# Kernel optimization log

Hardware: AMD Instinct MI355X
Metric: run time of the kernel (lower is better)

## Reference

```python
import jax, jax.numpy as jnp
import numpy as np

EPS_LN = 1e-5
EPS_SUM = 1e-5


def setup_inputs() -> dict:
    key = jax.random.key(0)
    ks = jax.random.split(key, 6)
    B, T, F, D = 8, 1024, 512, 64
    x = jax.random.normal(ks[0], (B, T, F), dtype=jnp.float32)
    state = jnp.zeros((B, 1, D * D), dtype=jnp.float32)
    s = 1.0 / np.sqrt(F)
    Wk = jax.random.uniform(ks[1], (F, D), jnp.float32, -s, s)
    Wq = jax.random.uniform(ks[2], (F, D), jnp.float32, -s, s)
    Wv = jax.random.uniform(ks[3], (F, D), jnp.float32, -s, s)
    gamma = jnp.ones((F,), jnp.float32)
    beta = jnp.zeros((F,), jnp.float32)
    return {"x": x, "state": state, "Wk": Wk, "Wq": Wq, "Wv": Wv,
            "gamma": gamma, "beta": beta}


def _layernorm(x, gamma, beta):
    mu = jnp.mean(x, axis=-1, keepdims=True)
    var = jnp.mean(jnp.square(x - mu), axis=-1, keepdims=True)
    return (x - mu) * jax.lax.rsqrt(var + EPS_LN) * gamma + beta


def reference(x, state, Wk, Wq, Wv, gamma, beta):
    B, T, F = x.shape
    D = Wk.shape[1]
    xn = _layernorm(x, gamma, beta)
    K = jax.nn.relu(xn @ Wk)            # [B,T,D]
    Q = jax.nn.relu(xn @ Wq)
    V = xn @ Wv
    # sum normalization (paper)
    K = K / (EPS_SUM + jnp.sum(K, axis=-1, keepdims=True))
    Q = Q / (EPS_SUM + jnp.sum(Q, axis=-1, keepdims=True))
    # outer-product fast weights per step: kv[b,t,i,j] = V[b,t,i] * K[b,t,j]
    kv = jnp.einsum('bti,btj->btij', V, K)        # [B,T,D,D]
    # 'sum' aggregator: running (cumulative) sum seeded by the initial state
    state_seq = state.reshape(B, 1, D, D) + jnp.cumsum(kv, axis=1)  # [B,T,D,D]
    y = jnp.einsum('btij,bti->btj', state_seq, Q)  # [B,T,D]
    return (y, state_seq)
```

## Files before the change

kernel.cpp:

```cpp
#include <hip/hip_runtime.h>

#define BB 8
#define TT 1024
#define FF 512
#define DD 64
#define LCH 16
#define CCH (TT / LCH)
#define SEG 8
#define NSEG (CCH / SEG)
#define EE (DD * DD)
#define NCT 12
#define AST 520
#define CST 196

typedef short short8 __attribute__((ext_vector_type(8)));
typedef float f32x4 __attribute__((ext_vector_type(4)));

__device__ __forceinline__ float wave_sum64(float v) {
  #pragma unroll
  for (int m = 32; m >= 1; m >>= 1) v += __shfl_xor(v, m, 64);
  return v;
}

__device__ __forceinline__ unsigned short f2bf(float f) {
  unsigned int u = __float_as_uint(f);
  u += 0x7FFFu + ((u >> 16) & 1u);
  return (unsigned short)(u >> 16);
}
__device__ __forceinline__ float bf2f(unsigned short h) {
  return __uint_as_float(((unsigned int)h) << 16);
}

__global__ __launch_bounds__(64) void wprep_k(
    const float* __restrict__ Wk, const float* __restrict__ Wq,
    const float* __restrict__ Wv,
    unsigned short* __restrict__ Wh, unsigned short* __restrict__ Wl) {
  int blk = blockIdx.x;
  int ct = blk >> 4, kk = blk & 15;
  int lane = threadIdx.x;
  int p = ct >> 2;
  const float* Wp = (p == 0) ? Wk : (p == 1) ? Wq : Wv;
  int d = ((ct & 3) << 4) + (lane & 15);
  int k0 = (kk << 5) + ((lane >> 4) << 3);
  size_t o = ((size_t)blk * 64 + lane) * 8;
  #pragma unroll
  for (int j = 0; j < 8; ++j) {
    float w = Wp[(size_t)(k0 + j) * DD + d];
    unsigned short h = f2bf(w);
    float rem = w - bf2f(h);
    Wh[o + j] = h;
    Wl[o + j] = f2bf(rem);
  }
}

__global__ __launch_bounds__(256) void lnprojcs_k(
    const float* __restrict__ x,
    const float* __restrict__ gamma, const float* __restrict__ beta,
    const unsigned short* __restrict__ Wh, const unsigned short* __restrict__ Wl,
    float* __restrict__ Ko, float* __restrict__ Qo, float* __restrict__ Vo,
    float* __restrict__ S) {
  __shared__ __align__(16) char smem[2 * LCH * AST * 2];
  unsigned short* lxh = (unsigned short*)smem;
  unsigned short* lxl = lxh + LCH * AST;
  float* lkqv = (float*)smem;

  const int tid = threadIdx.x;
  const int wv = tid >> 6, lane = tid & 63;
  const int bc = blockIdx.x;
  const size_t row0 = (size_t)bc * LCH;

  {
    float g[8], bt[8];
    #pragma unroll
    for (int k = 0; k < 8; ++k) {
      g[k]  = gamma[lane + 64 * k];
      bt[k] = beta[lane + 64 * k];
    }
    #pragma unroll
    for (int rr = 0; rr < 4; ++rr) {
      int r = wv * 4 + rr;
      const float* xr = x + (row0 + r) * FF;
      float v[8];
      float s = 0.f, ss = 0.f;
      #pragma unroll
      for (int k = 0; k < 8; ++k) {
        v[k] = xr[lane + 64 * k];
        s += v[k]; ss += v[k] * v[k];
      }
      s = wave_sum64(s); ss = wave_sum64(ss);
      float m = s * (1.f / FF);
      float var = ss * (1.f / FF) - m * m;
      float rs = rsqrtf(var + 1e-5f);
      #pragma unroll
      for (int k = 0; k < 8; ++k) {
        float xv = (v[k] - m) * rs * g[k] + bt[k];
        unsigned short h = f2bf(xv);
        float rem = xv - bf2f(h);
        lxh[r * AST + lane + 64 * k] = h;
        lxl[r * AST + lane + 64 * k] = f2bf(rem);
      }
    }
  }
  __syncthreads();

  f32x4 acc0 = {0.f, 0.f, 0.f, 0.f};
  f32x4 acc1 = {0.f, 0.f, 0.f, 0.f};
  f32x4 acc2 = {0.f, 0.f, 0.f, 0.f};
  {
    const int arow = lane & 15, agrp = lane >> 4;
    const unsigned short* abase = lxh + arow * AST + agrp * 8;
    const size_t wbase = (((size_t)(wv * 3) * 16) * 64 + lane) * 8;
    for (int kk = 0; kk < 16; ++kk) {
      const unsigned short* ap = abase + kk * 32;
      short8 ah = *(const short8*)ap;
      short8 al = *(const short8*)(ap + LCH * AST);
      size_t wo = wbase + (size_t)kk * 64 * 8;
      short8 bh0 = *(const short8*)(Wh + wo);
      short8 bl0 = *(const short8*)(Wl + wo);
      short8 bh1 = *(const short8*)(Wh + wo + 8192);
      short8 bl1 = *(const short8*)(Wl + wo + 8192);
      short8 bh2 = *(const short8*)(Wh + wo + 16384);
      short8 bl2 = *(const short8*)(Wl + wo + 16384);
      acc0 = __builtin_amdgcn_mfma_f32_16x16x32_bf16(ah, bh0, acc0, 0, 0, 0);
      acc0 = __builtin_amdgcn_mfma_f32_16x16x32_bf16(ah, bl0, acc0, 0, 0, 0);
      acc0 = __builtin_amdgcn_mfma_f32_16x16x32_bf16(al, bh0, acc0, 0, 0, 0);
      acc0 = __builtin_amdgcn_mfma_f32_16x16x32_bf16(al, bl0, acc0, 0, 0, 0);
      acc1 = __builtin_amdgcn_mfma_f32_16x16x32_bf16(ah, bh1, acc1, 0, 0, 0);
      acc1 = __builtin_amdgcn_mfma_f32_16x16x32_bf16(ah, bl1, acc1, 0, 0, 0);
      acc1 = __builtin_amdgcn_mfma_f32_16x16x32_bf16(al, bh1, acc1, 0, 0, 0);
      acc1 = __builtin_amdgcn_mfma_f32_16x16x32_bf16(al, bl1, acc1, 0, 0, 0);
      acc2 = __builtin_amdgcn_mfma_f32_16x16x32_bf16(ah, bh2, acc2, 0, 0, 0);
      acc2 = __builtin_amdgcn_mfma_f32_16x16x32_bf16(ah, bl2, acc2, 0, 0, 0);
      acc2 = __builtin_amdgcn_mfma_f32_16x16x32_bf16(al, bh2, acc2, 0, 0, 0);
      acc2 = __builtin_amdgcn_mfma_f32_16x16x32_bf16(al, bl2, acc2, 0, 0, 0);
    }
  }
  __syncthreads();

  {
    const int ccol = lane & 15, crow0 = (lane >> 4) << 2;
    const int n0 = (wv * 3) << 4;
    #pragma unroll
    for (int reg = 0; reg < 4; ++reg) {
      lkqv[(crow0 + reg) * CST + n0 +  0 + ccol] = acc0[reg];
      lkqv[(crow0 + reg) * CST + n0 + 16 + ccol] = acc1[reg];
      lkqv[(crow0 + reg) * CST + n0 + 32 + ccol] = acc2[reg];
    }
  }
  __syncthreads();

  #pragma unroll
  for (int i = 0; i < 12; ++i) {
    int pid = wv * 12 + i;
    int r = pid / 3, p = pid - r * 3;
    float val = lkqv[r * CST + p * 64 + lane];
    if (p < 2) {
      val = fmaxf(val, 0.f);
      float sm = wave_sum64(val);
      val = val / (1e-5f + sm);
    }
    float* outp = (p == 0) ? Ko : (p == 1) ? Qo : Vo;
    outp[(row0 + r) * DD + lane] = val;
    lkqv[r * CST + p * 64 + lane] = val;
  }
  __syncthreads();

  {
    const int j = lane, s0i = wv << 4;
    float a2[16];
    #pragma unroll
    for (int ii = 0; ii < 16; ++ii) a2[ii] = 0.f;
    #pragma unroll
    for (int t = 0; t < LCH; ++t) {
      float kj = lkqv[t * CST + j];
      #pragma unroll
      for (int ii = 0; ii < 16; ++ii)
        a2[ii] += lkqv[t * CST + 128 + s0i + ii] * kj;
    }
    float* Sp = S + (size_t)bc * EE;
    #pragma unroll
    for (int ii = 0; ii < 16; ++ii) Sp[(s0i + ii) * DD + j] = a2[ii];
  }
}

__global__ __launch_bounds__(256) void segsum_k(const float* __restrict__ S,
                                                float* __restrict__ Z) {
  int blk = blockIdx.x;
  int b = blk >> 7;
  int seg = (blk >> 4) & 7;
  int e = ((blk & 15) << 8) + threadIdx.x;
  const float* Sb = S + ((size_t)(b * CCH + seg * SEG)) * EE + e;
  float sv[SEG];
  #pragma unroll
  for (int c = 0; c < SEG; ++c) sv[c] = Sb[(size_t)c * EE];
  float acc = 0.f;
  #pragma unroll
  for (int c = 0; c < SEG; ++c) acc += sv[c];
  Z[((size_t)(b * NSEG + seg)) * EE + e] = acc;
}

__global__ __launch_bounds__(256) void segscan_k(const float* __restrict__ S,
                                                 const float* __restrict__ Z,
                                                 const float* __restrict__ st0,
                                                 float* __restrict__ P) {
  int blk = blockIdx.x;
  int b = blk >> 7;
  int seg = (blk >> 4) & 7;
  int e = ((blk & 15) << 8) + threadIdx.x;
  float run = st0[(size_t)b * EE + e];
  const float* Zb = Z + (size_t)b * NSEG * EE + e;
  float zv[NSEG - 1];
  #pragma unroll
  for (int s = 0; s < NSEG - 1; ++s) zv[s] = Zb[(size_t)s * EE];
  #pragma unroll
  for (int s = 0; s < NSEG - 1; ++s) if (s < seg) run += zv[s];
  const float* Sb = S + ((size_t)(b * CCH + seg * SEG)) * EE + e;
  float* Pb = P + ((size_t)(b * CCH + seg * SEG)) * EE + e;
  float sv[SEG];
  #pragma unroll
  for (int c = 0; c < SEG; ++c) sv[c] = Sb[(size_t)c * EE];
  #pragma unroll
  for (int c = 0; c < SEG; ++c) {
    Pb[(size_t)c * EE] = run;
    run += sv[c];
  }
}

__global__ __launch_bounds__(256) void scan_k(const float* __restrict__ Kx,
                     const float* __restrict__ Qx, const float* __restrict__ Vx,
                     const float* __restrict__ P,
                     float* __restrict__ y, float* __restrict__ sout) {
  int bc = blockIdx.x, tid = threadIdx.x;
  int wv = tid >> 6, j = tid & 63;
  int i0 = wv * 16;
  __shared__ float yp[4][LCH][DD];
  float Sr[16];
  const float* Pp = P + (size_t)bc * EE;
  #pragma unroll
  for (int ii = 0; ii < 16; ++ii) Sr[ii] = Pp[(i0 + ii) * DD + j];
  const float* Kb = Kx + (size_t)bc * LCH * DD;
  const float* Vb = Vx + (size_t)bc * LCH * DD;
  const float* Qb = Qx + (size_t)bc * LCH * DD;
  float kreg[LCH];
  #pragma unroll
  for (int t = 0; t < LCH; ++t) kreg[t] = Kb[t * DD + j];
  float* so = sout + (size_t)bc * LCH * EE + (size_t)i0 * DD + j;
  for (int t = 0; t < LCH; ++t) {
    const float* Vt = Vb + t * DD + i0;
    const float* Qt = Qb + t * DD + i0;
    float kj = kreg[t];
    float y0 = 0.f, y1 = 0.f, y2 = 0.f, y3 = 0.f;
    float* sot = so + (size_t)t * EE;
    #pragma unroll
    for (int ii = 0; ii < 16; ii += 4) {
      Sr[ii]     += Vt[ii]     * kj; sot[(ii)     * DD] = Sr[ii];     y0 += Sr[ii]     * Qt[ii];
      Sr[ii + 1] += Vt[ii + 1] * kj; sot[(ii + 1) * DD] = Sr[ii + 1]; y1 += Sr[ii + 1] * Qt[ii + 1];
      Sr[ii + 2] += Vt[ii + 2] * kj; sot[(ii + 2) * DD] = Sr[ii + 2]; y2 += Sr[ii + 2] * Qt[ii + 2];
      Sr[ii + 3] += Vt[ii + 3] * kj; sot[(ii + 3) * DD] = Sr[ii + 3]; y3 += Sr[ii + 3] * Qt[ii + 3];
    }
    yp[wv][t][j] = (y0 + y1) + (y2 + y3);
  }
  __syncthreads();
  float* yo = y + (size_t)bc * LCH * DD;
  #pragma unroll
  for (int tt = 0; tt < LCH / 4; ++tt) {
    int t = wv * (LCH / 4) + tt;
    yo[t * DD + j] = (yp[0][t][j] + yp[1][t][j]) + (yp[2][t][j] + yp[3][t][j]);
  }
}

extern "C" void kernel_launch(void* const* d_in, const int* in_sizes, int n_in,
                              void* d_out, int out_size, void* d_ws, size_t ws_size,
                              hipStream_t stream) {
  const float* x     = (const float*)d_in[0];
  const float* st0   = (const float*)d_in[1];
  const float* Wk    = (const float*)d_in[2];
  const float* Wq    = (const float*)d_in[3];
  const float* Wv    = (const float*)d_in[4];
  const float* gamma = (const float*)d_in[5];
  const float* beta  = (const float*)d_in[6];

  float* out  = (float*)d_out;
  float* yout = out;
  float* sseq = out + (size_t)BB * TT * DD;

  float* ws = (float*)d_ws;
  float* Ko = ws;
  float* Qo = Ko + (size_t)BB * TT * DD;
  float* Vo = Qo + (size_t)BB * TT * DD;
  float* S  = Vo + (size_t)BB * TT * DD;
  float* P  = S  + (size_t)BB * CCH * EE;
  float* Z  = P  + (size_t)BB * CCH * EE;
  unsigned short* Wh = (unsigned short*)(Z + (size_t)BB * NSEG * EE);
  unsigned short* Wl = Wh + (size_t)NCT * 16 * 64 * 8;

  wprep_k   <<<NCT * 16, 64, 0, stream>>>(Wk, Wq, Wv, Wh, Wl);
  lnprojcs_k<<<BB * CCH, 256, 0, stream>>>(x, gamma, beta, Wh, Wl, Ko, Qo, Vo, S);
  segsum_k  <<<BB * NSEG * 16, 256, 0, stream>>>(S, Z);
  segscan_k <<<BB * NSEG * 16, 256, 0, stream>>>(S, Z, st0, P);
  scan_k    <<<BB * CCH, 256, 0, stream>>>(Ko, Qo, Vo, P, yout, sseq);
}
```

Baseline: 187.9 us.

## Merge segment sum and scan kernels, widen scan blocks, use nontemporal stores

Replaces the two-pass segment-sum plus segment-scan pair with one kernel in which each block directly sums all preceding chunk states before writing its prefixes. This removes a launch and the Z buffer at the cost of redundant reads of earlier chunks, which grow with segment index. The scan kernel moves to 512 threads so each wave owns 8 rows instead of 16, and the large state_seq output is written with nontemporal stores to limit cache pollution.

```diff
diff --git a/kernel.cpp b/kernel.cpp
--- a/kernel.cpp
+++ b/kernel.cpp
@@ -183,42 +183,29 @@
   }
 }
 
-__global__ __launch_bounds__(256) void segsum_k(const float* __restrict__ S,
-                                                float* __restrict__ Z) {
+__global__ __launch_bounds__(256) void allprefix_k(const float* __restrict__ S,
+                                                   const float* __restrict__ st0,
+                                                   float* __restrict__ P) {
   int blk = blockIdx.x;
   int b = blk >> 7;
   int seg = (blk >> 4) & 7;
   int e = ((blk & 15) << 8) + threadIdx.x;
-  const float* Sb = S + ((size_t)(b * CCH + seg * SEG)) * EE + e;
+  const float* Sb = S + (size_t)b * CCH * EE + e;
+  float run = st0[(size_t)b * EE + e];
+  const int nprev = seg * SEG;
+  float r0 = 0.f, r1 = 0.f, r2 = 0.f, r3 = 0.f;
+  for (int c = 0; c < nprev; c += 4) {
+    r0 += Sb[(size_t)(c + 0) * EE];
+    r1 += Sb[(size_t)(c + 1) * EE];
+    r2 += Sb[(size_t)(c + 2) * EE];
+    r3 += Sb[(size_t)(c + 3) * EE];
+  }
+  run += (r0 + r1) + (r2 + r3);
+  const float* Ss = Sb + (size_t)nprev * EE;
   float sv[SEG];
   #pragma unroll
-  for (int c = 0; c < SEG; ++c) sv[c] = Sb[(size_t)c * EE];
-  float acc = 0.f;
-  #pragma unroll
-  for (int c = 0; c < SEG; ++c) acc += sv[c];
-  Z[((size_t)(b * NSEG + seg)) * EE + e] = acc;
-}
-
-__global__ __launch_bounds__(256) void segscan_k(const float* __restrict__ S,
-                                                 const float* __restrict__ Z,
-                                                 const float* __restrict__ st0,
-                                                 float* __restrict__ P) {
-  int blk = blockIdx.x;
-  int b = blk >> 7;
-  int seg = (blk >> 4) & 7;
-  int e = ((blk & 15) << 8) + threadIdx.x;
-  float run = st0[(size_t)b * EE + e];
-  const float* Zb = Z + (size_t)b * NSEG * EE + e;
-  float zv[NSEG - 1];
-  #pragma unroll
-  for (int s = 0; s < NSEG - 1; ++s) zv[s] = Zb[(size_t)s * EE];
-  #pragma unroll
-  for (int s = 0; s < NSEG - 1; ++s) if (s < seg) run += zv[s];
-  const float* Sb = S + ((size_t)(b * CCH + seg * SEG)) * EE + e;
-  float* Pb = P + ((size_t)(b * CCH + seg * SEG)) * EE + e;
-  float sv[SEG];
-  #pragma unroll
-  for (int c = 0; c < SEG; ++c) sv[c] = Sb[(size_t)c * EE];
+  for (int c = 0; c < SEG; ++c) sv[c] = Ss[(size_t)c * EE];
+  float* Pb = P + ((size_t)b * CCH + nprev) * EE + e;
   #pragma unroll
   for (int c = 0; c < SEG; ++c) {
     Pb[(size_t)c * EE] = run;
@@ -226,18 +213,18 @@
   }
 }
 
-__global__ __launch_bounds__(256) void scan_k(const float* __restrict__ Kx,
+__global__ __launch_bounds__(512) void scan_k(const float* __restrict__ Kx,
                      const float* __restrict__ Qx, const float* __restrict__ Vx,
                      const float* __restrict__ P,
                      float* __restrict__ y, float* __restrict__ sout) {
   int bc = blockIdx.x, tid = threadIdx.x;
   int wv = tid >> 6, j = tid & 63;
-  int i0 = wv * 16;
-  __shared__ float yp[4][LCH][DD];
-  float Sr[16];
+  int i0 = wv * 8;
+  __shared__ float yp[8][LCH][DD];
+  float Sr[8];
   const float* Pp = P + (size_t)bc * EE;
   #pragma unroll
-  for (int ii = 0; ii < 16; ++ii) Sr[ii] = Pp[(i0 + ii) * DD + j];
+  for (int ii = 0; ii < 8; ++ii) Sr[ii] = Pp[(i0 + ii) * DD + j];
   const float* Kb = Kx + (size_t)bc * LCH * DD;
   const float* Vb = Vx + (size_t)bc * LCH * DD;
   const float* Qb = Qx + (size_t)bc * LCH * DD;
@@ -252,20 +239,23 @@
     float y0 = 0.f, y1 = 0.f, y2 = 0.f, y3 = 0.f;
     float* sot = so + (size_t)t * EE;
     #pragma unroll
-    for (int ii = 0; ii < 16; ii += 4) {
-      Sr[ii]     += Vt[ii]     * kj; sot[(ii)     * DD] = Sr[ii];     y0 += Sr[ii]     * Qt[ii];
-      Sr[ii + 1] += Vt[ii + 1] * kj; sot[(ii + 1) * DD] = Sr[ii + 1]; y1 += Sr[ii + 1] * Qt[ii + 1];
-      Sr[ii + 2] += Vt[ii + 2] * kj; sot[(ii + 2) * DD] = Sr[ii + 2]; y2 += Sr[ii + 2] * Qt[ii + 2];
-      Sr[ii + 3] += Vt[ii + 3] * kj; sot[(ii + 3) * DD] = Sr[ii + 3]; y3 += Sr[ii + 3] * Qt[ii + 3];
+    for (int ii = 0; ii < 8; ii += 4) {
+      Sr[ii]     += Vt[ii]     * kj; __builtin_nontemporal_store(Sr[ii],     &sot[(ii)     * DD]); y0 += Sr[ii]     * Qt[ii];
+      Sr[ii + 1] += Vt[ii + 1] * kj; __builtin_nontemporal_store(Sr[ii + 1], &sot[(ii + 1) * DD]); y1 += Sr[ii + 1] * Qt[ii + 1];
+      Sr[ii + 2] += Vt[ii + 2] * kj; __builtin_nontemporal_store(Sr[ii + 2], &sot[(ii + 2) * DD]); y2 += Sr[ii + 2] * Qt[ii + 2];
+      Sr[ii + 3] += Vt[ii + 3] * kj; __builtin_nontemporal_store(Sr[ii + 3], &sot[(ii + 3) * DD]); y3 += Sr[ii + 3] * Qt[ii + 3];
     }
     yp[wv][t][j] = (y0 + y1) + (y2 + y3);
   }
   __syncthreads();
   float* yo = y + (size_t)bc * LCH * DD;
   #pragma unroll
-  for (int tt = 0; tt < LCH / 4; ++tt) {
-    int t = wv * (LCH / 4) + tt;
-    yo[t * DD + j] = (yp[0][t][j] + yp[1][t][j]) + (yp[2][t][j] + yp[3][t][j]);
+  for (int tt = 0; tt < LCH / 8; ++tt) {
+    int t = wv * (LCH / 8) + tt;
+    float v = 0.f;
+    #pragma unroll
+    for (int w = 0; w < 8; ++w) v += yp[w][t][j];
+    yo[t * DD + j] = v;
   }
 }
 
@@ -290,13 +280,11 @@
   float* Vo = Qo + (size_t)BB * TT * DD;
   float* S  = Vo + (size_t)BB * TT * DD;
   float* P  = S  + (size_t)BB * CCH * EE;
-  float* Z  = P  + (size_t)BB * CCH * EE;
-  unsigned short* Wh = (unsigned short*)(Z + (size_t)BB * NSEG * EE);
+  unsigned short* Wh = (unsigned short*)(P + (size_t)BB * CCH * EE);
   unsigned short* Wl = Wh + (size_t)NCT * 16 * 64 * 8;
 
-  wprep_k   <<<NCT * 16, 64, 0, stream>>>(Wk, Wq, Wv, Wh, Wl);
-  lnprojcs_k<<<BB * CCH, 256, 0, stream>>>(x, gamma, beta, Wh, Wl, Ko, Qo, Vo, S);
-  segsum_k  <<<BB * NSEG * 16, 256, 0, stream>>>(S, Z);
-  segscan_k <<<BB * NSEG * 16, 256, 0, stream>>>(S, Z, st0, P);
-  scan_k    <<<BB * CCH, 256, 0, stream>>>(Ko, Qo, Vo, P, yout, sseq);
-}
+  wprep_k    <<<NCT * 16, 64, 0, stream>>>(Wk, Wq, Wv, Wh, Wl);
+  lnprojcs_k <<<BB * CCH, 256, 0, stream>>>(x, gamma, beta, Wh, Wl, Ko, Qo, Vo, S);
+  allprefix_k<<<BB * NSEG * 16, 256, 0, stream>>>(S, st0, P);
+  scan_k     <<<BB * CCH, 512, 0, stream>>>(Ko, Qo, Vo, P, yout, sseq);
+}
```

Result: slower. 192.1 us (+2.2%).
